# Optimization experiments

Measured on AMD Instinct MI355X. Metric: run time of the kernel, lower is better.

The kernel has to match this reference:

```python
import jax, jax.numpy as jnp
import numpy as np

N = 10000
E = 160000
DIMS = [512, 512, 512, 256]  # in -> hidden -> hidden -> out (num_layers=3)
EPS = 1e-12  # F.normalize default eps


def _sage_layer(x, edge_index, Wl, b, Wr):
    # PyG SAGEConv (mean aggr, normalize=True):
    # out = lin_l(mean_{j in N(i)} x_j) + lin_r(x_i), then L2-normalize rows.
    src = edge_index[0]
    dst = edge_index[1]
    msg = x[src]  # [E, d] gather of source-node features
    agg = jax.ops.segment_sum(msg, dst, num_segments=N)  # [N, d]
    cnt = jax.ops.segment_sum(jnp.ones((E,), x.dtype), dst, num_segments=N)
    mean = agg / jnp.maximum(cnt, 1.0)[:, None]
    out = mean @ Wl.T + b + x @ Wr.T
    norm = jnp.sqrt(jnp.sum(out * out, axis=-1, keepdims=True))
    return out / jnp.maximum(norm, EPS)


def setup_inputs() -> dict:
    key = jax.random.key(0)
    ks = jax.random.split(key, 2 + 3 * len(DIMS))
    x = jax.random.normal(ks[0], (N, DIMS[0]), dtype=jnp.float32)
    edge_index = jax.random.randint(ks[1], (2, E), 0, N, dtype=jnp.int64)
    inp = {"x": x, "edge_index": edge_index}
    k = 2
    for i in range(len(DIMS) - 1):
        din, dout = DIMS[i], DIMS[i + 1]
        s = 1.0 / np.sqrt(din)
        inp[f"Wl{i}"] = jax.random.uniform(ks[k], (dout, din), jnp.float32, -s, s); k += 1
        inp[f"b{i}"] = jax.random.uniform(ks[k], (dout,), jnp.float32, -s, s); k += 1
        inp[f"Wr{i}"] = jax.random.uniform(ks[k], (dout, din), jnp.float32, -s, s); k += 1
    return inp


def reference(x, edge_index, Wl0, b0, Wr0, Wl1, b1, Wr1, Wl2, b2, Wr2):
    params = [(Wl0, b0, Wr0), (Wl1, b1, Wr1), (Wl2, b2, Wr2)]
    for Wl, b, Wr in params:
        x = _sage_layer(x, edge_index, Wl, b, Wr)
        x = jax.nn.relu(x)
        # F.dropout(training=False) is identity at inference
    return x
```

## Files before the change

### kernel.cpp

```cpp
#include <hip/hip_runtime.h>

#define NN 10000

typedef __attribute__((ext_vector_type(8))) short short8;
typedef __attribute__((ext_vector_type(4))) float f32x4;
typedef __attribute__((ext_vector_type(8))) _Float16 h16x8;
typedef __attribute__((ext_vector_type(4))) _Float16 h16x4;

__device__ __forceinline__ ushort f2b(float f) {
    union { float f; uint32_t u; } v; v.f = f;
    uint32_t u = v.u;
    return (ushort)((u + 0x7fffu + ((u >> 16) & 1u)) >> 16);
}
__device__ __forceinline__ uint packbf(float a, float b) {
    return (uint)f2b(a) | ((uint)f2b(b) << 16);
}
__device__ __forceinline__ float blo(uint u) {
    union { uint u; float f; } v; v.u = u << 16; return v.f;
}
__device__ __forceinline__ float bhi(uint u) {
    union { uint u; float f; } v; v.u = u & 0xffff0000u; return v.f;
}

__global__ __launch_bounds__(256) void count_dst(const int* __restrict__ dst,
                                                 int* __restrict__ counts, int E) {
    int i = blockIdx.x * 256 + threadIdx.x;
    if (i < E) atomicAdd(&counts[dst[i]], 1);
}

__global__ __launch_bounds__(1024) void scan_build(const int* __restrict__ counts,
                                                   int* __restrict__ offsets,
                                                   int* __restrict__ cursor,
                                                   float* __restrict__ inv_cnt, int n) {
    __shared__ int part[1024];
    int tid = threadIdx.x;
    int per = (n + 1023) / 1024;
    int base = tid * per;
    int s = 0;
    for (int i = 0; i < per; i++) { int idx = base + i; if (idx < n) s += counts[idx]; }
    part[tid] = s;
    __syncthreads();
    for (int off = 1; off < 1024; off <<= 1) {
        int v = (tid >= off) ? part[tid - off] : 0;
        __syncthreads();
        part[tid] += v;
        __syncthreads();
    }
    int run = (tid > 0) ? part[tid - 1] : 0;
    for (int i = 0; i < per; i++) {
        int idx = base + i;
        if (idx < n) {
            int c = counts[idx];
            offsets[idx] = run;
            cursor[idx]  = run;
            inv_cnt[idx] = 1.0f / fmaxf((float)c, 1.0f);
            run += c;
        }
    }
}

__global__ __launch_bounds__(256) void scatter_edges(const int* __restrict__ src,
                                                     const int* __restrict__ dst,
                                                     int* __restrict__ cursor,
                                                     int* __restrict__ sorted_src, int E) {
    int i = blockIdx.x * 256 + threadIdx.x;
    if (i < E) {
        int p = atomicAdd(&cursor[dst[i]], 1);
        sorted_src[p] = src[i];
    }
}

__global__ __launch_bounds__(256) void cvt_all(const float* __restrict__ x,
                                               const float* __restrict__ Wl0,
                                               const float* __restrict__ Wr0,
                                               const float* __restrict__ Wl1,
                                               const float* __restrict__ Wr1,
                                               const float* __restrict__ Wl2,
                                               const float* __restrict__ Wr2,
                                               ushort* __restrict__ xbuf,
                                               ushort* __restrict__ Wc0,
                                               ushort* __restrict__ Wc1,
                                               ushort* __restrict__ Wc2,
                                               int* __restrict__ counts) {
    int i = blockIdx.x * 256 + threadIdx.x;
    const float* src;
    ushort* dst;
    if (i < 1280000) {
        int idx = i * 4;
        src = x + idx;
        dst = xbuf + idx;
    } else if (i < 1411072) {
        int j = (i - 1280000) * 4;
        int row = j >> 9, col = j & 511;
        src = (row < 512) ? (Wl0 + (size_t)row * 512 + col)
                          : (Wr0 + (size_t)(row - 512) * 512 + col);
        dst = Wc0 + j;
    } else if (i < 1542144) {
        int j = (i - 1411072) * 4;
        int row = j >> 9, col = j & 511;
        src = (row < 512) ? (Wl1 + (size_t)row * 512 + col)
                          : (Wr1 + (size_t)(row - 512) * 512 + col);
        dst = Wc1 + j;
    } else if (i < 1607680) {
        int j = (i - 1542144) * 4;
        int row = j >> 9, col = j & 511;
        src = (row < 256) ? (Wl2 + (size_t)row * 512 + col)
                          : (Wr2 + (size_t)(row - 256) * 512 + col);
        dst = Wc2 + j;
    } else if (i < 1610180) {
        int t = i - 1607680;
        int4 z = {0, 0, 0, 0};
        *(int4*)(counts + t * 4) = z;
        return;
    } else {
        return;
    }
    float4 v = *(const float4*)src;
    uint2 p;
    p.x = packbf(v.x, v.y);
    p.y = packbf(v.z, v.w);
    *(uint2*)dst = p;
}

__global__ __launch_bounds__(256) void gemm_split(const ushort* __restrict__ A,
                                                  const ushort* __restrict__ B,
                                                  ushort* __restrict__ G,
                                                  _Float16* __restrict__ R,
                                                  int M, int dout) {
    __shared__ ushort Asl[2][128 * 32];
    __shared__ ushort Bsl[2][128 * 32];
    const int tid  = threadIdx.x;
    const int w    = tid >> 6;
    const int lane = tid & 63;

    const int nbx = gridDim.x, nby = gridDim.y;
    const int nwg = nbx * nby;
    const int id  = blockIdx.y * nbx + blockIdx.x;
    const int qq  = nwg >> 3, rr = nwg & 7;
    const int xcd = id & 7, blk = id >> 3;
    const int swzid = (xcd < rr ? xcd * (qq + 1) : rr * (qq + 1) + (xcd - rr) * qq) + blk;
    const int bx = swzid % nbx, by = swzid / nbx;

    const int bm = by * 128, bn = bx * 128;
    const int wm = (w & 1) * 64, wn = (w >> 1) * 64;
    const int row16 = lane & 15, q = lane >> 4;

    f32x4 acc[4][4];
#pragma unroll
    for (int i = 0; i < 4; i++)
#pragma unroll
        for (int j = 0; j < 4; j++) acc[i][j] = (f32x4){0.f, 0.f, 0.f, 0.f};

    const int sc_r = lane >> 2;
    const int sc_s = lane & 3;
    const int koff = sc_s ^ ((sc_r >> 1) & 3);
    const int swz  = (row16 >> 1) & 3;

    auto stage = [&](int buf, int k0) {
#pragma unroll
        for (int c = 0; c < 2; c++) {
            int chunk = w * 2 + c;
            int rloc  = chunk * 16 + sc_r;
            int growA = bm + rloc; growA = growA < M ? growA : M - 1;
            const ushort* gpA = A + (size_t)growA * 512 + k0 + koff * 8;
            __builtin_amdgcn_global_load_lds(
                (const __attribute__((address_space(1))) uint32_t*)gpA,
                (__attribute__((address_space(3))) uint32_t*)&Asl[buf][chunk * 512],
                16, 0, 0);
            const ushort* gpB = B + (size_t)(bn + rloc) * 512 + k0 + koff * 8;
            __builtin_amdgcn_global_load_lds(
                (const __attribute__((address_space(1))) uint32_t*)gpB,
                (__attribute__((address_space(3))) uint32_t*)&Bsl[buf][chunk * 512],
                16, 0, 0);
        }
    };

    const int NT = 512 / 32;
    stage(0, 0);
    __syncthreads();
    int cur = 0;

    for (int t = 0; t < NT; ++t) {
        if (t + 1 < NT) stage(cur ^ 1, (t + 1) * 32);

        short8 af[4], bfr[4];
        int s = q ^ swz;
#pragma unroll
        for (int i = 0; i < 4; i++) {
            int r = wm + i * 16 + row16;
            af[i] = *(const short8*)&Asl[cur][r * 32 + s * 8];
        }
#pragma unroll
        for (int j = 0; j < 4; j++) {
            int rn = wn + j * 16 + row16;
            bfr[j] = *(const short8*)&Bsl[cur][rn * 32 + s * 8];
        }
#pragma unroll
        for (int i = 0; i < 4; i++)
#pragma unroll
            for (int j = 0; j < 4; j++)
                acc[i][j] = __builtin_amdgcn_mfma_f32_16x16x32_bf16(
                    af[i], bfr[j], acc[i][j], 0, 0, 0);

        __syncthreads();
        cur ^= 1;
    }

    const bool isR = (bn >= dout);
#pragma unroll
    for (int i = 0; i < 4; i++) {
#pragma unroll
        for (int r2 = 0; r2 < 4; r2++) {
            int row = bm + wm + i * 16 + q * 4 + r2;
            if (row < M) {
                if (isR) {
                    _Float16* Rp = R + (size_t)row * dout + (bn - dout) + wn + row16;
#pragma unroll
                    for (int j = 0; j < 4; j++)
                        Rp[j * 16] = (_Float16)acc[i][j][r2];
                } else {
                    ushort* Gp = G + (size_t)row * dout + bn + wn + row16;
#pragma unroll
                    for (int j = 0; j < 4; j++)
                        Gp[j * 16] = f2b(acc[i][j][r2]);
                }
            }
        }
    }
}

template <int DOUT, bool FINAL>
__global__ __launch_bounds__(256) void aggfin(const ushort* __restrict__ G,
                                              const _Float16* __restrict__ R,
                                              const float* __restrict__ bias,
                                              const int* __restrict__ offsets,
                                              const int* __restrict__ counts,
                                              const int* __restrict__ sorted_src,
                                              const float* __restrict__ inv_cnt,
                                              ushort* __restrict__ xnext,
                                              float* __restrict__ outf, int n) {
    constexpr int PL = DOUT / 64;
    int wave = threadIdx.x >> 6;
    int lane = threadIdx.x & 63;
    int node = blockIdx.x * 4 + wave;
    if (node >= n) return;
    int start = offsets[node];
    int cnt   = counts[node];
    float inv = inv_cnt[node];

    float acc[PL];
#pragma unroll
    for (int k = 0; k < PL; k++) acc[k] = 0.f;

    if constexpr (DOUT == 512) {
        const uint* gp = (const uint*)G + lane * 4;
#define ACC8(v) do { \
        acc[0] += blo(v.x); acc[1] += bhi(v.x); \
        acc[2] += blo(v.y); acc[3] += bhi(v.y); \
        acc[4] += blo(v.z); acc[5] += bhi(v.z); \
        acc[6] += blo(v.w); acc[7] += bhi(v.w); } while (0)
        int e = 0;
        for (; e + 8 <= cnt; e += 8) {
            uint4 vv[8];
#pragma unroll
            for (int u = 0; u < 8; u++) {
                int s0 = sorted_src[start + e + u];
                vv[u] = *(const uint4*)(gp + (size_t)s0 * 256);
            }
#pragma unroll
            for (int u = 0; u < 8; u++) ACC8(vv[u]);
        }
        for (; e < cnt; e++) {
            int s0 = sorted_src[start + e];
            uint4 v0 = *(const uint4*)(gp + (size_t)s0 * 256);
            ACC8(v0);
        }
#undef ACC8
    } else {
        const uint* gp = (const uint*)G + lane * 2;
#define ACC4(v) do { \
        acc[0] += blo(v.x); acc[1] += bhi(v.x); \
        acc[2] += blo(v.y); acc[3] += bhi(v.y); } while (0)
        int e = 0;
        for (; e + 8 <= cnt; e += 8) {
            uint2 vv[8];
#pragma unroll
            for (int u = 0; u < 8; u++) {
                int s0 = sorted_src[start + e + u];
                vv[u] = *(const uint2*)(gp + (size_t)s0 * 128);
            }
#pragma unroll
            for (int u = 0; u < 8; u++) ACC4(vv[u]);
        }
        for (; e < cnt; e++) {
            int s0 = sorted_src[start + e];
            uint2 v0 = *(const uint2*)(gp + (size_t)s0 * 128);
            ACC4(v0);
        }
#undef ACC4
    }

    float v[PL];
    const _Float16* Rp = R + (size_t)node * DOUT + lane * PL;
    const float* Bp = bias + lane * PL;
    if constexpr (PL == 8) {
        h16x8 hv = *(const h16x8*)Rp;
#pragma unroll
        for (int k = 0; k < PL; k += 4) {
            float4 b4 = *(const float4*)(Bp + k);
            v[k + 0] = acc[k + 0] * inv + (float)hv[k + 0] + b4.x;
            v[k + 1] = acc[k + 1] * inv + (float)hv[k + 1] + b4.y;
            v[k + 2] = acc[k + 2] * inv + (float)hv[k + 2] + b4.z;
            v[k + 3] = acc[k + 3] * inv + (float)hv[k + 3] + b4.w;
        }
    } else {
        h16x4 hv = *(const h16x4*)Rp;
#pragma unroll
        for (int k = 0; k < PL; k += 4) {
            float4 b4 = *(const float4*)(Bp + k);
            v[k + 0] = acc[k + 0] * inv + (float)hv[k + 0] + b4.x;
            v[k + 1] = acc[k + 1] * inv + (float)hv[k + 1] + b4.y;
            v[k + 2] = acc[k + 2] * inv + (float)hv[k + 2] + b4.z;
            v[k + 3] = acc[k + 3] * inv + (float)hv[k + 3] + b4.w;
        }
    }

    float ss = 0.f;
#pragma unroll
    for (int k = 0; k < PL; k++) ss += v[k] * v[k];
#pragma unroll
    for (int m = 32; m >= 1; m >>= 1) ss += __shfl_xor(ss, m, 64);
    float scale = 1.0f / fmaxf(sqrtf(ss), 1e-12f);

    if constexpr (FINAL) {
        float* Op = outf + (size_t)node * DOUT + lane * PL;
#pragma unroll
        for (int k = 0; k < PL; k += 4) {
            float4 o;
            o.x = fmaxf(v[k + 0] * scale, 0.f);
            o.y = fmaxf(v[k + 1] * scale, 0.f);
            o.z = fmaxf(v[k + 2] * scale, 0.f);
            o.w = fmaxf(v[k + 3] * scale, 0.f);
            *(float4*)(Op + k) = o;
        }
    } else {
        uint4 o;
        float r0 = fmaxf(v[0] * scale, 0.f), r1 = fmaxf(v[1] * scale, 0.f);
        float r2 = fmaxf(v[2] * scale, 0.f), r3 = fmaxf(v[3] * scale, 0.f);
        float r4 = fmaxf(v[4] * scale, 0.f), r5 = fmaxf(v[5] * scale, 0.f);
        float r6 = fmaxf(v[6] * scale, 0.f), r7 = fmaxf(v[7] * scale, 0.f);
        o.x = packbf(r0, r1); o.y = packbf(r2, r3);
        o.z = packbf(r4, r5); o.w = packbf(r6, r7);
        *(uint4*)(xnext + (size_t)node * 512 + lane * 8) = o;
    }
}

extern "C" void kernel_launch(void* const* d_in, const int* in_sizes, int n_in,
                              void* d_out, int out_size, void* d_ws, size_t ws_size,
                              hipStream_t stream) {
    const float* x    = (const float*)d_in[0];
    const int*   edge = (const int*)d_in[1];
    const float* Wl0  = (const float*)d_in[2];
    const float* b0   = (const float*)d_in[3];
    const float* Wr0  = (const float*)d_in[4];
    const float* Wl1  = (const float*)d_in[5];
    const float* b1   = (const float*)d_in[6];
    const float* Wr1  = (const float*)d_in[7];
    const float* Wl2  = (const float*)d_in[8];
    const float* b2   = (const float*)d_in[9];
    const float* Wr2  = (const float*)d_in[10];

    const int E = in_sizes[1] / 2;

    char* ws = (char*)d_ws;
    int*      counts  = (int*)(ws + 0);
    int*      offsets = (int*)(ws + 40960);
    int*      cursor  = (int*)(ws + 81920);
    float*    invc    = (float*)(ws + 122880);
    int*      sorted  = (int*)(ws + 163840);
    ushort*   Wc0     = (ushort*)(ws + 819200);
    ushort*   Wc1     = (ushort*)(ws + 1867776);
    ushort*   Wc2     = (ushort*)(ws + 2916352);
    ushort*   xbuf    = (ushort*)(ws + 3440640);
    ushort*   Gbuf    = (ushort*)(ws + 13680640);
    _Float16* Rbuf    = (_Float16*)(ws + 23920640);

    cvt_all<<<(1610180 + 255) / 256, 256, 0, stream>>>(x, Wl0, Wr0, Wl1, Wr1, Wl2, Wr2,
                                                       xbuf, Wc0, Wc1, Wc2, counts);

    count_dst<<<(E + 255) / 256, 256, 0, stream>>>(edge + E, counts, E);
    scan_build<<<1, 1024, 0, stream>>>(counts, offsets, cursor, invc, NN);
    scatter_edges<<<(E + 255) / 256, 256, 0, stream>>>(edge, edge + E, cursor, sorted, E);

    const int gyM = (NN + 127) / 128;
    const int gb  = (NN + 3) / 4;

    gemm_split<<<dim3(8, gyM), 256, 0, stream>>>(xbuf, Wc0, Gbuf, Rbuf, NN, 512);
    aggfin<512, false><<<gb, 256, 0, stream>>>(Gbuf, Rbuf, b0, offsets, counts,
                                               sorted, invc, xbuf, nullptr, NN);
    gemm_split<<<dim3(8, gyM), 256, 0, stream>>>(xbuf, Wc1, Gbuf, Rbuf, NN, 512);
    aggfin<512, false><<<gb, 256, 0, stream>>>(Gbuf, Rbuf, b1, offsets, counts,
                                               sorted, invc, xbuf, nullptr, NN);
    gemm_split<<<dim3(4, gyM), 256, 0, stream>>>(xbuf, Wc2, Gbuf, Rbuf, NN, 256);
    aggfin<256, true><<<gb, 256, 0, stream>>>(Gbuf, Rbuf, b2, offsets, counts,
                                              sorted, invc, nullptr, (float*)d_out, NN);
}
```

Before: 248.7 us.

## Split neighbor aggregation into column slices with atomic norm accumulation

```diff
diff --git a/kernel.cpp b/kernel.cpp
--- a/kernel.cpp
+++ b/kernel.cpp
@@ -81,7 +81,8 @@
                                                ushort* __restrict__ Wc0,
                                                ushort* __restrict__ Wc1,
                                                ushort* __restrict__ Wc2,
-                                               int* __restrict__ counts) {
+                                               int* __restrict__ counts,
+                                               float* __restrict__ ssq) {
     int i = blockIdx.x * 256 + threadIdx.x;
     const float* src;
     ushort* dst;
@@ -112,6 +113,11 @@
         int4 z = {0, 0, 0, 0};
         *(int4*)(counts + t * 4) = z;
         return;
+    } else if (i < 1612680) {
+        int t = i - 1610180;
+        float4 z = {0.f, 0.f, 0.f, 0.f};
+        *(float4*)(ssq + t * 4) = z;
+        return;
     } else {
         return;
     }
@@ -229,129 +235,101 @@
     }
 }
 
+template <int DOUT, bool F32V>
+__global__ __launch_bounds__(256) void slice_agg(const ushort* __restrict__ G,
+                                                 const _Float16* __restrict__ R,
+                                                 const float* __restrict__ bias,
+                                                 const int* __restrict__ offsets,
+                                                 const int* __restrict__ counts,
+                                                 const int* __restrict__ sorted_src,
+                                                 const float* __restrict__ inv_cnt,
+                                                 void* __restrict__ Vout,
+                                                 float* __restrict__ ssq, int n) {
+    constexpr int NSL = DOUT / 128;
+    int id    = blockIdx.x;
+    int slice = id & (NSL - 1);
+    int wave  = threadIdx.x >> 6;
+    int lane  = threadIdx.x & 63;
+    int node  = (id / NSL) * 4 + wave;
+    if (node >= n) return;
+    int start = offsets[node];
+    int cnt   = counts[node];
+
+    const uint* gp = (const uint*)G + slice * 64 + lane;
+    float a0 = 0.f, a1 = 0.f;
+    int e = 0;
+    for (; e + 8 <= cnt; e += 8) {
+        uint vv[8];
+#pragma unroll
+        for (int u = 0; u < 8; u++) {
+            int s0 = sorted_src[start + e + u];
+            vv[u] = gp[(size_t)s0 * (DOUT / 2)];
+        }
+#pragma unroll
+        for (int u = 0; u < 8; u++) { a0 += blo(vv[u]); a1 += bhi(vv[u]); }
+    }
+    for (; e < cnt; e++) {
+        int s0 = sorted_src[start + e];
+        uint v0 = gp[(size_t)s0 * (DOUT / 2)];
+        a0 += blo(v0); a1 += bhi(v0);
+    }
+
+    float inv  = inv_cnt[node];
+    int   colf = slice * 128 + lane * 2;
+    union { uint u; _Float16 h[2]; } hu;
+    hu.u = *(const uint*)(R + (size_t)node * DOUT + colf);
+    float2 b2 = *(const float2*)(bias + colf);
+    float v0 = a0 * inv + (float)hu.h[0] + b2.x;
+    float v1 = a1 * inv + (float)hu.h[1] + b2.y;
+
+    if constexpr (F32V) {
+        float2 o = {v0, v1};
+        *(float2*)((float*)Vout + (size_t)node * DOUT + colf) = o;
+    } else {
+        union { uint u; _Float16 h[2]; } ou;
+        ou.h[0] = (_Float16)v0; ou.h[1] = (_Float16)v1;
+        *(uint*)((_Float16*)Vout + (size_t)node * DOUT + colf) = ou.u;
+    }
+
+    float ss = v0 * v0 + v1 * v1;
+#pragma unroll
+    for (int m = 32; m >= 1; m >>= 1) ss += __shfl_xor(ss, m, 64);
+    if (lane == 0) atomicAdd(&ssq[node], ss);
+}
+
 template <int DOUT, bool FINAL>
-__global__ __launch_bounds__(256) void aggfin(const ushort* __restrict__ G,
-                                              const _Float16* __restrict__ R,
-                                              const float* __restrict__ bias,
-                                              const int* __restrict__ offsets,
-                                              const int* __restrict__ counts,
-                                              const int* __restrict__ sorted_src,
-                                              const float* __restrict__ inv_cnt,
-                                              ushort* __restrict__ xnext,
-                                              float* __restrict__ outf, int n) {
-    constexpr int PL = DOUT / 64;
+__global__ __launch_bounds__(256) void norm_fin(const void* __restrict__ Vin,
+                                                float* __restrict__ ssq,
+                                                ushort* __restrict__ xnext,
+                                                float* __restrict__ outf, int n) {
     int wave = threadIdx.x >> 6;
     int lane = threadIdx.x & 63;
     int node = blockIdx.x * 4 + wave;
     if (node >= n) return;
-    int start = offsets[node];
-    int cnt   = counts[node];
-    float inv = inv_cnt[node];
-
-    float acc[PL];
-#pragma unroll
-    for (int k = 0; k < PL; k++) acc[k] = 0.f;
-
-    if constexpr (DOUT == 512) {
-        const uint* gp = (const uint*)G + lane * 4;
-#define ACC8(v) do { \
-        acc[0] += blo(v.x); acc[1] += bhi(v.x); \
-        acc[2] += blo(v.y); acc[3] += bhi(v.y); \
-        acc[4] += blo(v.z); acc[5] += bhi(v.z); \
-        acc[6] += blo(v.w); acc[7] += bhi(v.w); } while (0)
-        int e = 0;
-        for (; e + 8 <= cnt; e += 8) {
-            uint4 vv[8];
-#pragma unroll
-            for (int u = 0; u < 8; u++) {
-                int s0 = sorted_src[start + e + u];
-                vv[u] = *(const uint4*)(gp + (size_t)s0 * 256);
-            }
-#pragma unroll
-            for (int u = 0; u < 8; u++) ACC8(vv[u]);
-        }
-        for (; e < cnt; e++) {
-            int s0 = sorted_src[start + e];
-            uint4 v0 = *(const uint4*)(gp + (size_t)s0 * 256);
-            ACC8(v0);
-        }
-#undef ACC8
-    } else {
-        const uint* gp = (const uint*)G + lane * 2;
-#define ACC4(v) do { \
-        acc[0] += blo(v.x); acc[1] += bhi(v.x); \
-        acc[2] += blo(v.y); acc[3] += bhi(v.y); } while (0)
-        int e = 0;
-        for (; e + 8 <= cnt; e += 8) {
-            uint2 vv[8];
-#pragma unroll
-            for (int u = 0; u < 8; u++) {
-                int s0 = sorted_src[start + e + u];
-                vv[u] = *(const uint2*)(gp + (size_t)s0 * 128);
-            }
-#pragma unroll
-            for (int u = 0; u < 8; u++) ACC4(vv[u]);
-        }
-        for (; e < cnt; e++) {
-            int s0 = sorted_src[start + e];
-            uint2 v0 = *(const uint2*)(gp + (size_t)s0 * 128);
-            ACC4(v0);
-        }
-#undef ACC4
-    }
-
-    float v[PL];
-    const _Float16* Rp = R + (size_t)node * DOUT + lane * PL;
-    const float* Bp = bias + lane * PL;
-    if constexpr (PL == 8) {
-        h16x8 hv = *(const h16x8*)Rp;
-#pragma unroll
-        for (int k = 0; k < PL; k += 4) {
-            float4 b4 = *(const float4*)(Bp + k);
-            v[k + 0] = acc[k + 0] * inv + (float)hv[k + 0] + b4.x;
-            v[k + 1] = acc[k + 1] * inv + (float)hv[k + 1] + b4.y;
-            v[k + 2] = acc[k + 2] * inv + (float)hv[k + 2] + b4.z;
-            v[k + 3] = acc[k + 3] * inv + (float)hv[k + 3] + b4.w;
-        }
-    } else {
-        h16x4 hv = *(const h16x4*)Rp;
-#pragma unroll
-        for (int k = 0; k < PL; k += 4) {
-            float4 b4 = *(const float4*)(Bp + k);
-            v[k + 0] = acc[k + 0] * inv + (float)hv[k + 0] + b4.x;
-            v[k + 1] = acc[k + 1] * inv + (float)hv[k + 1] + b4.y;
-            v[k + 2] = acc[k + 2] * inv + (float)hv[k + 2] + b4.z;
-            v[k + 3] = acc[k + 3] * inv + (float)hv[k + 3] + b4.w;
-        }
-    }
-
-    float ss = 0.f;
-#pragma unroll
-    for (int k = 0; k < PL; k++) ss += v[k] * v[k];
-#pragma unroll
-    for (int m = 32; m >= 1; m >>= 1) ss += __shfl_xor(ss, m, 64);
+    float ss = ssq[node];
     float scale = 1.0f / fmaxf(sqrtf(ss), 1e-12f);
 
-    if constexpr (FINAL) {
-        float* Op = outf + (size_t)node * DOUT + lane * PL;
-#pragma unroll
-        for (int k = 0; k < PL; k += 4) {
-            float4 o;
-            o.x = fmaxf(v[k + 0] * scale, 0.f);
-            o.y = fmaxf(v[k + 1] * scale, 0.f);
-            o.z = fmaxf(v[k + 2] * scale, 0.f);
-            o.w = fmaxf(v[k + 3] * scale, 0.f);
-            *(float4*)(Op + k) = o;
-        }
-    } else {
+    if constexpr (!FINAL) {
+        const _Float16* Vp = (const _Float16*)Vin + (size_t)node * DOUT + lane * 8;
+        h16x8 hv = *(const h16x8*)Vp;
+        float r0 = fmaxf((float)hv[0] * scale, 0.f), r1 = fmaxf((float)hv[1] * scale, 0.f);
+        float r2 = fmaxf((float)hv[2] * scale, 0.f), r3 = fmaxf((float)hv[3] * scale, 0.f);
+        float r4 = fmaxf((float)hv[4] * scale, 0.f), r5 = fmaxf((float)hv[5] * scale, 0.f);
+        float r6 = fmaxf((float)hv[6] * scale, 0.f), r7 = fmaxf((float)hv[7] * scale, 0.f);
         uint4 o;
-        float r0 = fmaxf(v[0] * scale, 0.f), r1 = fmaxf(v[1] * scale, 0.f);
-        float r2 = fmaxf(v[2] * scale, 0.f), r3 = fmaxf(v[3] * scale, 0.f);
-        float r4 = fmaxf(v[4] * scale, 0.f), r5 = fmaxf(v[5] * scale, 0.f);
-        float r6 = fmaxf(v[6] * scale, 0.f), r7 = fmaxf(v[7] * scale, 0.f);
         o.x = packbf(r0, r1); o.y = packbf(r2, r3);
         o.z = packbf(r4, r5); o.w = packbf(r6, r7);
         *(uint4*)(xnext + (size_t)node * 512 + lane * 8) = o;
+        if (lane == 0) ssq[node] = 0.f;
+    } else {
+        const float* Vp = (const float*)Vin + (size_t)node * DOUT + lane * 4;
+        float4 vv = *(const float4*)Vp;
+        float4 o;
+        o.x = fmaxf(vv.x * scale, 0.f);
+        o.y = fmaxf(vv.y * scale, 0.f);
+        o.z = fmaxf(vv.z * scale, 0.f);
+        o.w = fmaxf(vv.w * scale, 0.f);
+        *(float4*)(outf + (size_t)node * DOUT + lane * 4) = o;
     }
 }
 
@@ -384,9 +362,11 @@
     ushort*   xbuf    = (ushort*)(ws + 3440640);
     ushort*   Gbuf    = (ushort*)(ws + 13680640);
     _Float16* Rbuf    = (_Float16*)(ws + 23920640);
-
-    cvt_all<<<(1610180 + 255) / 256, 256, 0, stream>>>(x, Wl0, Wr0, Wl1, Wr1, Wl2, Wr2,
-                                                       xbuf, Wc0, Wc1, Wc2, counts);
+    void*     Vbuf    = (void*)(ws + 34160640);
+    float*    ssq     = (float*)(ws + 44400640);
+
+    cvt_all<<<(1612680 + 255) / 256, 256, 0, stream>>>(x, Wl0, Wr0, Wl1, Wr1, Wl2, Wr2,
+                                                       xbuf, Wc0, Wc1, Wc2, counts, ssq);
 
     count_dst<<<(E + 255) / 256, 256, 0, stream>>>(edge + E, counts, E);
     scan_build<<<1, 1024, 0, stream>>>(counts, offsets, cursor, invc, NN);
@@ -396,12 +376,15 @@
     const int gb  = (NN + 3) / 4;
 
     gemm_split<<<dim3(8, gyM), 256, 0, stream>>>(xbuf, Wc0, Gbuf, Rbuf, NN, 512);
-    aggfin<512, false><<<gb, 256, 0, stream>>>(Gbuf, Rbuf, b0, offsets, counts,
-                                               sorted, invc, xbuf, nullptr, NN);
+    slice_agg<512, false><<<gb * 4, 256, 0, stream>>>(Gbuf, Rbuf, b0, offsets, counts,
+                                                      sorted, invc, Vbuf, ssq, NN);
+    norm_fin<512, false><<<gb, 256, 0, stream>>>(Vbuf, ssq, xbuf, nullptr, NN);
     gemm_split<<<dim3(8, gyM), 256, 0, stream>>>(xbuf, Wc1, Gbuf, Rbuf, NN, 512);
-    aggfin<512, false><<<gb, 256, 0, stream>>>(Gbuf, Rbuf, b1, offsets, counts,
-                                               sorted, invc, xbuf, nullptr, NN);
+    slice_agg<512, false><<<gb * 4, 256, 0, stream>>>(Gbuf, Rbuf, b1, offsets, counts,
+                                                      sorted, invc, Vbuf, ssq, NN);
+    norm_fin<512, false><<<gb, 256, 0, stream>>>(Vbuf, ssq, xbuf, nullptr, NN);
     gemm_split<<<dim3(4, gyM), 256, 0, stream>>>(xbuf, Wc2, Gbuf, Rbuf, NN, 256);
-    aggfin<256, true><<<gb, 256, 0, stream>>>(Gbuf, Rbuf, b2, offsets, counts,
-                                              sorted, invc, nullptr, (float*)d_out, NN);
-}
+    slice_agg<256, true><<<gb * 2, 256, 0, stream>>>(Gbuf, Rbuf, b2, offsets, counts,
+                                                     sorted, invc, Vbuf, ssq, NN);
+    norm_fin<256, true><<<gb, 256, 0, stream>>>(Vbuf, ssq, nullptr, (float*)d_out, NN);
+}
```

Result: slower. 275.3 us (+10.7%).
